# Optimization experiments

Hardware: AMD Instinct MI355X
Metric: run time of the kernel (lower is better)

Reference implementation:

```python
import jax, jax.numpy as jnp
import numpy as np

N_HEADS = 16

def setup_inputs() -> dict:
    key = jax.random.key(0)
    ks = jax.random.split(key, 5)
    B, T, C = 4, 2048, 1024
    x = jax.random.normal(ks[0], (B, T, C), dtype=jnp.float32)
    w_qkv = jax.random.normal(ks[1], (C, 3 * C), dtype=jnp.float32) * (C ** -0.5)
    b_qkv = jnp.zeros((3 * C,), dtype=jnp.float32)
    w_proj = jax.random.normal(ks[2], (C, C), dtype=jnp.float32) * (C ** -0.5)
    b_proj = jnp.zeros((C,), dtype=jnp.float32)
    return {"x": x, "w_qkv": w_qkv, "b_qkv": b_qkv, "w_proj": w_proj, "b_proj": b_proj}


def reference(x, w_qkv, b_qkv, w_proj, b_proj):
    B, T, C = x.shape
    H = N_HEADS
    hd = C // H
    scale = hd ** -0.5
    qkv = x @ w_qkv + b_qkv                      # [B,T,3C]
    q, k, v = jnp.split(qkv, 3, axis=-1)         # each [B,T,C]
    # -> [B,H,T,hd]
    q = q.reshape(B, T, H, hd).transpose(0, 2, 1, 3)
    k = k.reshape(B, T, H, hd).transpose(0, 2, 1, 3)
    v = v.reshape(B, T, H, hd).transpose(0, 2, 1, 3)
    attn = jnp.einsum("bhqd,bhkd->bhqk", q, k) * scale
    causal = jnp.tril(jnp.ones((T, T), dtype=bool))
    attn = jnp.where(causal, attn, -jnp.inf)
    attn = jax.nn.softmax(attn, axis=-1)         # dropout p=0 in eval/reference
    out = jnp.einsum("bhqk,bhkd->bhqd", attn, v)
    out = out.transpose(0, 2, 1, 3).reshape(B, T, C)
    return out @ w_proj + b_proj
```

## Files before the change

kernel.cpp:

```cpp
#include <hip/hip_runtime.h>
#include <hip/hip_bf16.h>


typedef float f32x4 __attribute__((ext_vector_type(4)));
typedef float f32x16 __attribute__((ext_vector_type(16)));
typedef __bf16 bf16x8 __attribute__((ext_vector_type(8)));
typedef short short8v __attribute__((ext_vector_type(8)));
typedef unsigned int u32x4 __attribute__((ext_vector_type(4)));

__device__ __forceinline__ unsigned short f2bf(float f) {
  __hip_bfloat16 h = __float2bfloat16(f);
  return __builtin_bit_cast(unsigned short, h);
}

__device__ __forceinline__ void glds16(const void* g, void* l) {
  __builtin_amdgcn_global_load_lds((const __attribute__((address_space(1))) void*)g,
                                   (__attribute__((address_space(3))) void*)l, 16, 0, 0);
}

__global__ void cvt_f32_bf16_kernel(const float* __restrict__ in,
                                    unsigned short* __restrict__ out, int n) {
  int stride = gridDim.x * blockDim.x * 4;
  for (int i = (blockIdx.x * blockDim.x + threadIdx.x) * 4; i < n; i += stride) {
    float4 v = *(const float4*)(in + i);
    ushort4 o;
    o.x = f2bf(v.x); o.y = f2bf(v.y); o.z = f2bf(v.z); o.w = f2bf(v.w);
    *(ushort4*)(out + i) = o;
  }
}

__global__ void transpose_cvt_kernel(const float* __restrict__ in,
                                     unsigned short* __restrict__ out, int K, int N) {
  __shared__ unsigned short tile[32][33];
  int tx = threadIdx.x & 31, ty = threadIdx.x >> 5;
  int n0 = blockIdx.x * 32, k0 = blockIdx.y * 32;
#pragma unroll
  for (int i = 0; i < 32; i += 8)
    tile[ty + i][tx] = f2bf(in[(size_t)(k0 + ty + i) * N + n0 + tx]);
  __syncthreads();
#pragma unroll
  for (int i = 0; i < 32; i += 8)
    out[(size_t)(n0 + ty + i) * K + k0 + tx] = tile[tx][ty + i];
}

template <int OUT_F32>
__global__ __launch_bounds__(512, 2) void gemm_bt_kernel(
    const unsigned short* __restrict__ A, const unsigned short* __restrict__ Bt,
    const float* __restrict__ bias, void* __restrict__ Cv, int M, int N, int K) {
  __shared__ unsigned short sA[2][256 * 64];
  __shared__ unsigned short sB[2][256 * 64];
  int tid = threadIdx.x;
  int lane = tid & 63, wid = tid >> 6;
  int g = lane >> 4, r16 = lane & 15;

  int gx = gridDim.x;
  int bid = blockIdx.y * gx + blockIdx.x;
  int cpx = (gx * gridDim.y) >> 3;
  int nid = (bid & 7) * cpx + (bid >> 3);
  int m0 = (nid / gx) * 256, n0 = (nid % gx) * 256;

  int wm = wid >> 2, wn = wid & 3;
  f32x4 acc[8][4] = {};

  int nt = K >> 6;

  auto STAGE = [&](int buf, int kt) {
#pragma unroll
    for (int j = 0; j < 4; ++j) {
      int c = tid + j * 512;
      int row = c >> 3, slot = c & 7;
      int gcol = kt * 64 + (slot ^ (row & 7)) * 8;
      glds16(A + (size_t)(m0 + row) * K + gcol, &sA[buf][c * 8]);
      glds16(Bt + (size_t)(n0 + row) * K + gcol, &sB[buf][c * 8]);
    }
  };

  STAGE(0, 0);
  asm volatile("s_waitcnt vmcnt(0)" ::: "memory");
  __builtin_amdgcn_s_barrier();

  int cur = 0;
#pragma unroll 1
  for (int t = 0; t < nt; ++t) {
    if (t + 1 < nt) STAGE(cur ^ 1, t + 1);
    const unsigned short* a = sA[cur];
    const unsigned short* bb = sB[cur];
#pragma unroll
    for (int kk = 0; kk < 2; ++kk) {
      bf16x8 af[8], bf[4];
#pragma unroll
      for (int mf = 0; mf < 8; ++mf) {
        int r = wm * 128 + mf * 16 + r16;
        af[mf] = *(const bf16x8*)&a[r * 64 + (((kk * 4 + g) ^ (r & 7)) << 3)];
      }
#pragma unroll
      for (int nf = 0; nf < 4; ++nf) {
        int r = wn * 64 + nf * 16 + r16;
        bf[nf] = *(const bf16x8*)&bb[r * 64 + (((kk * 4 + g) ^ (r & 7)) << 3)];
      }
      __builtin_amdgcn_s_setprio(1);
#pragma unroll
      for (int mf = 0; mf < 8; ++mf)
#pragma unroll
        for (int nf = 0; nf < 4; ++nf)
          acc[mf][nf] = __builtin_amdgcn_mfma_f32_16x16x32_bf16(af[mf], bf[nf], acc[mf][nf], 0, 0, 0);
      __builtin_amdgcn_s_setprio(0);
    }
    asm volatile("s_waitcnt vmcnt(0)" ::: "memory");
    __builtin_amdgcn_s_barrier();
    cur ^= 1;
  }

#pragma unroll
  for (int mf = 0; mf < 8; ++mf)
#pragma unroll
    for (int nf = 0; nf < 4; ++nf)
#pragma unroll
      for (int r = 0; r < 4; ++r) {
        int row = m0 + wm * 128 + mf * 16 + g * 4 + r;
        int col = n0 + wn * 64 + nf * 16 + r16;
        float v = acc[mf][nf][r] + bias[col];
        if (OUT_F32)
          ((float*)Cv)[(size_t)row * N + col] = v;
        else
          ((unsigned short*)Cv)[(size_t)row * N + col] = f2bf(v);
      }
}

__global__ void transpose_v_kernel(const unsigned short* __restrict__ qkv,
                                   unsigned short* __restrict__ vT) {
  __shared__ unsigned short tl[64][80];
  int t0 = blockIdx.x * 64;
  int bh = blockIdx.y, b = bh >> 4, h = bh & 15;
  int tid = threadIdx.x;
  int row = tid >> 2, c0 = (tid & 3) * 16;
  const unsigned short* src =
      qkv + (size_t)(b * 2048 + t0 + row) * 3072 + 2048 + h * 64 + c0;
  short8v a0 = *(const short8v*)src;
  short8v a1 = *(const short8v*)(src + 8);
#pragma unroll
  for (int j = 0; j < 8; ++j) tl[c0 + j][row] = (unsigned short)a0[j];
#pragma unroll
  for (int j = 0; j < 8; ++j) tl[c0 + 8 + j][row] = (unsigned short)a1[j];
  __syncthreads();
  int dd = tid >> 2, tc = (tid & 3) * 16;
  unsigned short* dst = vT + (size_t)(bh * 64 + dd) * 2048 + t0 + tc;
  *(short8v*)dst = *(const short8v*)&tl[dd][tc];
  *(short8v*)(dst + 8) = *(const short8v*)&tl[dd][tc + 8];
}

__global__ __launch_bounds__(512, 4) void attn_kernel(
    const unsigned short* __restrict__ qkv, const unsigned short* __restrict__ vT,
    unsigned short* __restrict__ ao) {
  __shared__ unsigned short sK[2][4096];
  __shared__ unsigned short sV[2][4096];
  __shared__ float lbuf[8][32];
  const int T = 2048, C3 = 3072;
  const float K1 = 23.083120654223415f;
  const float K2 = 16158.66f;
  int x = blockIdx.x;
  int xcd = x & 7, rest = x >> 3;
  int bh = xcd * 8 + (rest & 7);
  int qt = 7 - (rest >> 3);
  int b = bh >> 4, h = bh & 15;
  int tid = threadIdx.x, lane = tid & 63, w = tid >> 6;
  int l31 = lane & 31, hi = lane >> 5;

  int c = tid;
  int row = c >> 3, oct = (c & 7) ^ (row & 7);
  const unsigned short* Kb = qkv + (size_t)(b * T + row) * C3 + 1024 + h * 64 + oct * 8;
  const unsigned short* Vb = vT + (size_t)(bh * 64 + row) * 2048 + oct * 8;

  auto STAGE = [&](int buf, int kt) {
    int kv0 = kt * 64;
    glds16(Kb + (size_t)kv0 * C3, &sK[buf][c * 8]);
    glds16(Vb + kv0, &sV[buf][c * 8]);
  };

  int wq0 = qt * 256 + w * 32;

  const unsigned short* qp = qkv + (size_t)(b * T + wq0 + l31) * C3 + h * 64;
  bf16x8 qf[4];
#pragma unroll
  for (int d0 = 0; d0 < 4; ++d0)
    qf[d0] = *(const bf16x8*)(qp + d0 * 16 + hi * 8);

  u32x4 onesw = {0x3F803F80u, 0x3F803F80u, 0x3F803F80u, 0x3F803F80u};
  bf16x8 vones = __builtin_bit_cast(bf16x8, onesw);

  f32x16 o[2] = {};
  f32x16 lacc = {};

  int nkv = 4 * qt + 4;
  STAGE(0, 0);
  __syncthreads();
  int cur = 0;
#pragma unroll 1
  for (int kt = 0; kt < nkv; ++kt) {
    if (kt + 1 < nkv) STAGE(cur ^ 1, kt + 1);
    int kv0 = kt * 64;
    if (kv0 <= wq0 + 31) {
      f32x16 s[2] = {};
      __builtin_amdgcn_s_setprio(1);
#pragma unroll
      for (int d0 = 0; d0 < 4; ++d0) {
        int oc = ((d0 * 2 + hi) ^ (l31 & 7)) * 8;
        bf16x8 kf0 = *(const bf16x8*)&sK[cur][l31 * 64 + oc];
        bf16x8 kf1 = *(const bf16x8*)&sK[cur][(32 + l31) * 64 + oc];
        s[0] = __builtin_amdgcn_mfma_f32_32x32x16_bf16(kf0, qf[d0], s[0], 0, 0, 0);
        s[1] = __builtin_amdgcn_mfma_f32_32x32x16_bf16(kf1, qf[d0], s[1], 0, 0, 0);
      }
      __builtin_amdgcn_s_setprio(0);

      if (kv0 + 63 > wq0) {
        int thr = wq0 + l31 - kv0 - 4 * hi;
#pragma unroll
        for (int sub = 0; sub < 2; ++sub)
#pragma unroll
          for (int r = 0; r < 16; ++r) {
            int cc = sub * 32 + (r & 3) + 8 * (r >> 2);
            s[sub][r] = (cc <= thr) ? s[sub][r] : -3e38f;
          }
      }

      int pb[2][16];
#pragma unroll
      for (int sub = 0; sub < 2; ++sub)
#pragma unroll
        for (int r = 0; r < 16; ++r)
          pb[sub][r] = (int)fmaxf(fmaf(s[sub][r], K1, K2), 0.0f);

      unsigned int pk[2][8];
#pragma unroll
      for (int sub = 0; sub < 2; ++sub)
#pragma unroll
        for (int i = 0; i < 8; ++i)
          pk[sub][i] = __builtin_amdgcn_perm((unsigned)pb[sub][2 * i + 1],
                                             (unsigned)pb[sub][2 * i], 0x05040100u);
      unsigned int rc[2][4];
#pragma unroll
      for (int sub = 0; sub < 2; ++sub) {
        unsigned int s0 = hi ? pk[sub][0] : pk[sub][2];
        unsigned int s1 = hi ? pk[sub][1] : pk[sub][3];
        unsigned int s2 = hi ? pk[sub][4] : pk[sub][6];
        unsigned int s3 = hi ? pk[sub][5] : pk[sub][7];
        rc[sub][0] = __shfl_xor(s0, 32, 64);
        rc[sub][1] = __shfl_xor(s1, 32, 64);
        rc[sub][2] = __shfl_xor(s2, 32, 64);
        rc[sub][3] = __shfl_xor(s3, 32, 64);
      }

      __builtin_amdgcn_s_setprio(1);
#pragma unroll
      for (int sub = 0; sub < 2; ++sub)
#pragma unroll
        for (int t = 0; t < 2; ++t) {
          u32x4 av;
          av.x = hi ? rc[sub][2 * t]     : pk[sub][4 * t];
          av.y = hi ? rc[sub][2 * t + 1] : pk[sub][4 * t + 1];
          av.z = hi ? pk[sub][4 * t + 2] : rc[sub][2 * t];
          av.w = hi ? pk[sub][4 * t + 3] : rc[sub][2 * t + 1];
          bf16x8 pa = __builtin_bit_cast(bf16x8, av);
          int kvs = sub * 2 + t;
          int ocv = ((kvs * 2 + hi) ^ (l31 & 7)) * 8;
          bf16x8 vf0 = *(const bf16x8*)&sV[cur][l31 * 64 + ocv];
          bf16x8 vf1 = *(const bf16x8*)&sV[cur][(32 + l31) * 64 + ocv];
          o[0] = __builtin_amdgcn_mfma_f32_32x32x16_bf16(pa, vf0, o[0], 0, 0, 0);
          o[1] = __builtin_amdgcn_mfma_f32_32x32x16_bf16(pa, vf1, o[1], 0, 0, 0);
          lacc = __builtin_amdgcn_mfma_f32_32x32x16_bf16(pa, vones, lacc, 0, 0, 0);
        }
      __builtin_amdgcn_s_setprio(0);
    }
    __syncthreads();
    cur ^= 1;
  }

  if (l31 == 0) {
#pragma unroll
    for (int r = 0; r < 16; ++r)
      lbuf[w][(r & 3) + 8 * (r >> 2) + 4 * hi] = lacc[r];
  }
  __syncthreads();
  float inv = 1.f / lbuf[w][l31];
#pragma unroll
  for (int r = 0; r < 16; ++r) {
    int qrow = (r & 3) + 8 * (r >> 2) + 4 * hi;
    float iv = __shfl(inv, qrow, 64);
    size_t base = (size_t)(b * T + wq0 + qrow) * 1024 + h * 64 + l31;
    ao[base] = f2bf(o[0][r] * iv);
    ao[base + 32] = f2bf(o[1][r] * iv);
  }
}

extern "C" void kernel_launch(void* const* d_in, const int* in_sizes, int n_in,
                              void* d_out, int out_size, void* d_ws, size_t ws_size,
                              hipStream_t stream) {
  const float* x      = (const float*)d_in[0];
  const float* w_qkv  = (const float*)d_in[1];
  const float* b_qkv  = (const float*)d_in[2];
  const float* w_proj = (const float*)d_in[3];
  const float* b_proj = (const float*)d_in[4];
  float* out = (float*)d_out;

  char* ws = (char*)d_ws;
  unsigned short* xb     = (unsigned short*)(ws);
  unsigned short* ao     = (unsigned short*)(ws);
  unsigned short* wqkvT  = (unsigned short*)(ws + (16u << 20));
  unsigned short* wprojT = (unsigned short*)(ws + (22u << 20));
  unsigned short* qkv    = (unsigned short*)(ws + (24u << 20));
  unsigned short* vT     = (unsigned short*)(ws + (72u << 20));

  cvt_f32_bf16_kernel<<<2048, 256, 0, stream>>>(x, xb, 8192 * 1024);
  transpose_cvt_kernel<<<dim3(3072 / 32, 1024 / 32), 256, 0, stream>>>(w_qkv, wqkvT, 1024, 3072);
  transpose_cvt_kernel<<<dim3(1024 / 32, 1024 / 32), 256, 0, stream>>>(w_proj, wprojT, 1024, 1024);

  gemm_bt_kernel<0><<<dim3(3072 / 256, 8192 / 256), 512, 0, stream>>>(
      xb, wqkvT, b_qkv, (void*)qkv, 8192, 3072, 1024);

  transpose_v_kernel<<<dim3(32, 64), 256, 0, stream>>>(qkv, vT);

  attn_kernel<<<dim3(512), 512, 0, stream>>>(qkv, vT, ao);

  gemm_bt_kernel<1><<<dim3(1024 / 256, 8192 / 256), 512, 0, stream>>>(
      ao, wprojT, b_proj, (void*)out, 8192, 1024, 1024);
}
```

Baseline: 191.6 us.

## Deepen GEMM pipeline to 4-stage BK=32 ring and narrow proj tile

The bf16 GEMM changes from a double-buffered BK=64 loop, which drained all loads each step, to a 4-slot ring of BK=32 tiles. Three tiles are kept in flight, and partial vmcnt waits plus one barrier per step replace the full drain. The output projection now uses a 256x128 tile, so it launches twice as many blocks on a 1024-wide output. The risks are lower occupancy from launch_bounds(512,1) and different shared-memory usage and swizzle.

```diff
diff --git a/kernel.cpp b/kernel.cpp
--- a/kernel.cpp
+++ b/kernel.cpp
@@ -16,6 +16,14 @@
 __device__ __forceinline__ void glds16(const void* g, void* l) {
   __builtin_amdgcn_global_load_lds((const __attribute__((address_space(1))) void*)g,
                                    (__attribute__((address_space(3))) void*)l, 16, 0, 0);
+}
+
+template <int N> __device__ __forceinline__ void waitvm() {
+  if constexpr (N == 0) asm volatile("s_waitcnt vmcnt(0)" ::: "memory");
+  else if constexpr (N == 3) asm volatile("s_waitcnt vmcnt(3)" ::: "memory");
+  else if constexpr (N == 4) asm volatile("s_waitcnt vmcnt(4)" ::: "memory");
+  else if constexpr (N == 6) asm volatile("s_waitcnt vmcnt(6)" ::: "memory");
+  else if constexpr (N == 8) asm volatile("s_waitcnt vmcnt(8)" ::: "memory");
 }
 
 __global__ void cvt_f32_bf16_kernel(const float* __restrict__ in,
@@ -43,12 +51,16 @@
     out[(size_t)(n0 + ty + i) * K + k0 + tx] = tile[tx][ty + i];
 }
 
-template <int OUT_F32>
-__global__ __launch_bounds__(512, 2) void gemm_bt_kernel(
+template <int OUT_F32, int BN>
+__global__ __launch_bounds__(512, 1) void gemm_bt_kernel(
     const unsigned short* __restrict__ A, const unsigned short* __restrict__ Bt,
     const float* __restrict__ bias, void* __restrict__ Cv, int M, int N, int K) {
-  __shared__ unsigned short sA[2][256 * 64];
-  __shared__ unsigned short sB[2][256 * 64];
+  constexpr int BM = 256;
+  constexpr int NPB = BN / 128;
+  constexpr int NL = 2 + NPB;
+  constexpr int NFN = BN / 64;
+  __shared__ unsigned short sA[4][BM * 32];
+  __shared__ unsigned short sB[4][BN * 32];
   int tid = threadIdx.x;
   int lane = tid & 63, wid = tid >> 6;
   int g = lane >> 4, r16 = lane & 15;
@@ -57,68 +69,76 @@
   int bid = blockIdx.y * gx + blockIdx.x;
   int cpx = (gx * gridDim.y) >> 3;
   int nid = (bid & 7) * cpx + (bid >> 3);
-  int m0 = (nid / gx) * 256, n0 = (nid % gx) * 256;
+  int m0 = (nid / gx) * BM, n0 = (nid % gx) * BN;
 
   int wm = wid >> 2, wn = wid & 3;
-  f32x4 acc[8][4] = {};
-
-  int nt = K >> 6;
-
-  auto STAGE = [&](int buf, int kt) {
-#pragma unroll
-    for (int j = 0; j < 4; ++j) {
-      int c = tid + j * 512;
-      int row = c >> 3, slot = c & 7;
-      int gcol = kt * 64 + (slot ^ (row & 7)) * 8;
-      glds16(A + (size_t)(m0 + row) * K + gcol, &sA[buf][c * 8]);
-      glds16(Bt + (size_t)(n0 + row) * K + gcol, &sB[buf][c * 8]);
+  f32x4 acc[8][NFN] = {};
+
+  auto STAGE = [&](int slot, int j) {
+    int k0 = j << 5;
+#pragma unroll
+    for (int p = 0; p < 2; ++p) {
+      int c = p * 512 + tid;
+      int row = c >> 2, sl = c & 3;
+      int sg = sl ^ ((row ^ (row >> 2)) & 3);
+      glds16(A + (size_t)(m0 + row) * K + k0 + sg * 8, &sA[slot][c * 8]);
+    }
+#pragma unroll
+    for (int p = 0; p < NPB; ++p) {
+      int c = p * 512 + tid;
+      int row = c >> 2, sl = c & 3;
+      int sg = sl ^ ((row ^ (row >> 2)) & 3);
+      glds16(Bt + (size_t)(n0 + row) * K + k0 + sg * 8, &sB[slot][c * 8]);
     }
   };
 
+  int NJ = K >> 5;
   STAGE(0, 0);
-  asm volatile("s_waitcnt vmcnt(0)" ::: "memory");
-  __builtin_amdgcn_s_barrier();
-
-  int cur = 0;
+  STAGE(1, 1);
+  STAGE(2, 2);
+
+  int swr = (r16 ^ (r16 >> 2)) & 3;
+  int oc = (g ^ swr) << 3;
+
 #pragma unroll 1
-  for (int t = 0; t < nt; ++t) {
-    if (t + 1 < nt) STAGE(cur ^ 1, t + 1);
-    const unsigned short* a = sA[cur];
-    const unsigned short* bb = sB[cur];
-#pragma unroll
-    for (int kk = 0; kk < 2; ++kk) {
-      bf16x8 af[8], bf[4];
-#pragma unroll
-      for (int mf = 0; mf < 8; ++mf) {
-        int r = wm * 128 + mf * 16 + r16;
-        af[mf] = *(const bf16x8*)&a[r * 64 + (((kk * 4 + g) ^ (r & 7)) << 3)];
-      }
-#pragma unroll
-      for (int nf = 0; nf < 4; ++nf) {
-        int r = wn * 64 + nf * 16 + r16;
-        bf[nf] = *(const bf16x8*)&bb[r * 64 + (((kk * 4 + g) ^ (r & 7)) << 3)];
-      }
+  for (int j = 0; j < NJ; ++j) {
+    if (j + 2 < NJ) waitvm<2 * NL>();
+    else if (j + 1 < NJ) waitvm<NL>();
+    else waitvm<0>();
+    __builtin_amdgcn_s_barrier();
+    __builtin_amdgcn_sched_barrier(0);
+    if (j + 3 < NJ) STAGE((j + 3) & 3, j + 3);
+    const unsigned short* a = sA[j & 3];
+    const unsigned short* bb = sB[j & 3];
+    bf16x8 bfr[NFN];
+#pragma unroll
+    for (int nf = 0; nf < NFN; ++nf)
+      bfr[nf] = *(const bf16x8*)&bb[((wn * (BN / 4) + nf * 16 + r16) << 5) + oc];
+#pragma unroll
+    for (int h = 0; h < 2; ++h) {
+      bf16x8 af[4];
+#pragma unroll
+      for (int mf = 0; mf < 4; ++mf)
+        af[mf] = *(const bf16x8*)&a[((wm * 128 + (h * 4 + mf) * 16 + r16) << 5) + oc];
       __builtin_amdgcn_s_setprio(1);
 #pragma unroll
-      for (int mf = 0; mf < 8; ++mf)
-#pragma unroll
-        for (int nf = 0; nf < 4; ++nf)
-          acc[mf][nf] = __builtin_amdgcn_mfma_f32_16x16x32_bf16(af[mf], bf[nf], acc[mf][nf], 0, 0, 0);
+      for (int mf = 0; mf < 4; ++mf)
+#pragma unroll
+        for (int nf = 0; nf < NFN; ++nf)
+          acc[h * 4 + mf][nf] =
+              __builtin_amdgcn_mfma_f32_16x16x32_bf16(af[mf], bfr[nf], acc[h * 4 + mf][nf], 0, 0, 0);
       __builtin_amdgcn_s_setprio(0);
     }
-    asm volatile("s_waitcnt vmcnt(0)" ::: "memory");
-    __builtin_amdgcn_s_barrier();
-    cur ^= 1;
   }
 
 #pragma unroll
   for (int mf = 0; mf < 8; ++mf)
 #pragma unroll
-    for (int nf = 0; nf < 4; ++nf)
+    for (int nf = 0; nf < NFN; ++nf)
 #pragma unroll
       for (int r = 0; r < 4; ++r) {
         int row = m0 + wm * 128 + mf * 16 + g * 4 + r;
-        int col = n0 + wn * 64 + nf * 16 + r16;
+        int col = n0 + wn * (BN / 4) + nf * 16 + r16;
         float v = acc[mf][nf][r] + bias[col];
         if (OUT_F32)
           ((float*)Cv)[(size_t)row * N + col] = v;
@@ -204,9 +224,9 @@
       __builtin_amdgcn_s_setprio(1);
 #pragma unroll
       for (int d0 = 0; d0 < 4; ++d0) {
-        int oc = ((d0 * 2 + hi) ^ (l31 & 7)) * 8;
-        bf16x8 kf0 = *(const bf16x8*)&sK[cur][l31 * 64 + oc];
-        bf16x8 kf1 = *(const bf16x8*)&sK[cur][(32 + l31) * 64 + oc];
+        int oc2 = ((d0 * 2 + hi) ^ (l31 & 7)) * 8;
+        bf16x8 kf0 = *(const bf16x8*)&sK[cur][l31 * 64 + oc2];
+        bf16x8 kf1 = *(const bf16x8*)&sK[cur][(32 + l31) * 64 + oc2];
         s[0] = __builtin_amdgcn_mfma_f32_32x32x16_bf16(kf0, qf[d0], s[0], 0, 0, 0);
         s[1] = __builtin_amdgcn_mfma_f32_32x32x16_bf16(kf1, qf[d0], s[1], 0, 0, 0);
       }
@@ -314,13 +334,13 @@
   transpose_cvt_kernel<<<dim3(3072 / 32, 1024 / 32), 256, 0, stream>>>(w_qkv, wqkvT, 1024, 3072);
   transpose_cvt_kernel<<<dim3(1024 / 32, 1024 / 32), 256, 0, stream>>>(w_proj, wprojT, 1024, 1024);
 
-  gemm_bt_kernel<0><<<dim3(3072 / 256, 8192 / 256), 512, 0, stream>>>(
+  gemm_bt_kernel<0, 256><<<dim3(3072 / 256, 8192 / 256), 512, 0, stream>>>(
       xb, wqkvT, b_qkv, (void*)qkv, 8192, 3072, 1024);
 
   transpose_v_kernel<<<dim3(32, 64), 256, 0, stream>>>(qkv, vT);
 
   attn_kernel<<<dim3(512), 512, 0, stream>>>(qkv, vT, ao);
 
-  gemm_bt_kernel<1><<<dim3(1024 / 256, 8192 / 256), 512, 0, stream>>>(
+  gemm_bt_kernel<1, 128><<<dim3(1024 / 128, 8192 / 256), 512, 0, stream>>>(
       ao, wprojT, b_proj, (void*)out, 8192, 1024, 1024);
 }
```

Result: slower. 200.1 us (+4.5%).
